# Kernel optimization log

Hardware: AMD Instinct MI355X
Metric: run time of the kernel (lower is better)

The kernel has to match this reference:

```python
import jax, jax.numpy as jnp
import numpy as np

EPS = 1e-6
B, T, D, A = 16, 2048, 512, 128
SCALE = A ** (-0.5)


def _xavier(key, fan_in, fan_out):
    limit = np.sqrt(6.0 / (fan_in + fan_out)).astype(np.float32)
    return jax.random.uniform(key, (fan_in, fan_out), jnp.float32, -limit, limit)


def setup_inputs() -> dict:
    key = jax.random.key(0)
    kx, kq, kk, kv = jax.random.split(key, 4)
    x = jax.random.normal(kx, (B, T, D), jnp.float32)
    Wq = _xavier(kq, D, A)
    Wk = _xavier(kk, D, A)
    Wv = _xavier(kv, D, 1)
    bq = jnp.full((A,), 0.01, jnp.float32)
    bk = jnp.full((A,), 0.01, jnp.float32)
    bv = jnp.full((1,), 0.01, jnp.float32)
    return {"x": x, "Wq": Wq, "bq": bq, "Wk": Wk, "bk": bk, "Wv": Wv, "bv": bv}


def reference(x, Wq, bq, Wk, bk, Wv, bv):
    # mean-variance norm over features (torch.std default is unbiased -> ddof=1)
    mu = jnp.mean(x, axis=-1, keepdims=True)
    sd = jnp.std(x, axis=-1, keepdims=True, ddof=1)
    xn = (x - mu) / (sd + EPS)
    Q = xn @ Wq + bq            # [B, T, A]
    K = xn @ Wk + bk            # [B, T, A]
    V = xn @ Wv + bv            # [B, T, 1]
    scores = jnp.einsum("bta,bsa->bts", Q, K) * SCALE  # [B, T, T]
    w_att = jax.nn.softmax(scores, axis=-1)
    w = jnp.einsum("bts,bso->bto", w_att, V)           # [B, T, 1]
    return (w, w_att)
```

## Files before the change

kernel.cpp:

```cpp
#include <hip/hip_runtime.h>

#define NB 16
#define NT 2048
#define ND 512
#define NA 128
#define EPSV 1e-6f
#define SCALE 0.08838834764831845f
#define NCH 4
#define SCH 512

typedef __bf16 bf16;
typedef __bf16 bf16x4 __attribute__((ext_vector_type(4)));
typedef __bf16 bf16x8 __attribute__((ext_vector_type(8)));
typedef float f32x4 __attribute__((ext_vector_type(4)));

__global__ void prep_wt(const float* __restrict__ Wq, const float* __restrict__ Wk,
                        bf16* __restrict__ WT) {
    int n = blockIdx.x;
    const float* W = (n < NA) ? Wq : Wk;
    int col = n & (NA - 1);
    for (int k = threadIdx.x; k < ND; k += blockDim.x)
        WT[(size_t)n * ND + k] = (bf16)W[(size_t)k * NA + col];
}

__launch_bounds__(256)
__global__ void norm_proj(const float* __restrict__ x, const float* __restrict__ Wv,
                          const float* __restrict__ bvp, const bf16* __restrict__ WT,
                          const float* __restrict__ bq, const float* __restrict__ bk,
                          bf16* __restrict__ QK, float* __restrict__ Vout) {
    __shared__ bf16 xn[16 * ND];
    const int tid = threadIdx.x;
    const int lane = tid & 63, wv = tid >> 6;
    const int row0 = blockIdx.x * 16;

    float wvv[8];
    float sumw = 0.f;
#pragma unroll
    for (int i = 0; i < 4; ++i) { wvv[i]     = Wv[lane * 4 + i];       sumw += wvv[i]; }
#pragma unroll
    for (int i = 0; i < 4; ++i) { wvv[4 + i] = Wv[256 + lane * 4 + i]; sumw += wvv[4 + i]; }
#pragma unroll
    for (int m = 1; m < 64; m <<= 1) sumw += __shfl_xor(sumw, m);
    const float bvs = bvp[0];

#pragma unroll
    for (int r = 0; r < 4; ++r) {
        const int lrow = wv * 4 + r;
        const int grow = row0 + lrow;
        const float* xr = x + (size_t)grow * ND;
        f32x4 a = *(const f32x4*)(xr + lane * 4);
        f32x4 b = *(const f32x4*)(xr + 256 + lane * 4);
        float s = 0.f, sq = 0.f, dw = 0.f;
#pragma unroll
        for (int i = 0; i < 4; ++i) { s += a[i]; sq += a[i] * a[i]; dw += a[i] * wvv[i]; }
#pragma unroll
        for (int i = 0; i < 4; ++i) { s += b[i]; sq += b[i] * b[i]; dw += b[i] * wvv[4 + i]; }
#pragma unroll
        for (int m = 1; m < 64; m <<= 1) {
            s  += __shfl_xor(s, m);
            sq += __shfl_xor(sq, m);
            dw += __shfl_xor(dw, m);
        }
        const float mu  = s * (1.f / 512.f);
        float var = (sq - 512.f * mu * mu) * (1.f / 511.f);
        var = fmaxf(var, 0.f);
        const float inv = 1.f / (sqrtf(var) + EPSV);
        if (lane == 0) Vout[grow] = (dw - mu * sumw) * inv + bvs;

        const int sw = (lrow & 7) << 4;
        bf16x4 v0, v1;
#pragma unroll
        for (int i = 0; i < 4; ++i) v0[i] = (bf16)((a[i] - mu) * inv);
#pragma unroll
        for (int i = 0; i < 4; ++i) v1[i] = (bf16)((b[i] - mu) * inv);
        *(bf16x4*)((char*)xn + lrow * 1024 + ((lane * 8) ^ sw))       = v0;
        *(bf16x4*)((char*)xn + lrow * 1024 + ((512 + lane * 8) ^ sw)) = v1;
    }
    __syncthreads();

    const int c = lane & 15, g = lane >> 4;
    const int asw = (c & 7) << 4;
    f32x4 acc[4];
#pragma unroll
    for (int i = 0; i < 4; ++i) acc[i] = f32x4{0.f, 0.f, 0.f, 0.f};

    for (int ks = 0; ks < 16; ++ks) {
        const bf16x8 af = *(const bf16x8*)((const char*)xn + c * 1024 +
                                           ((ks * 64 + g * 16) ^ asw));
#pragma unroll
        for (int i = 0; i < 4; ++i) {
            const int n = wv * 64 + i * 16 + c;
            const bf16x8 bfr = *(const bf16x8*)(WT + (size_t)n * ND + ks * 32 + g * 8);
            acc[i] = __builtin_amdgcn_mfma_f32_16x16x32_bf16(af, bfr, acc[i], 0, 0, 0);
        }
    }
#pragma unroll
    for (int i = 0; i < 4; ++i) {
        const int n = wv * 64 + i * 16 + c;
        const float bias = (n < NA) ? bq[n] : bk[n - NA];
#pragma unroll
        for (int j = 0; j < 4; ++j)
            QK[(size_t)(row0 + g * 4 + j) * 256 + n] = (bf16)(acc[i][j] + bias);
    }
}

__launch_bounds__(256, 3)
__global__ void attn_pass1(const bf16* __restrict__ QK, const float* __restrict__ Vg,
                           float* __restrict__ pl, float* __restrict__ pw) {
    __shared__ float redl[4][64], redw[4][64];
    const int tid = threadIdx.x;
    const int lane = tid & 63, w = tid >> 6;
    const int b = blockIdx.z, t0 = blockIdx.x * 64, sc = blockIdx.y;
    const int c = lane & 15, g = lane >> 4;

    bf16x8 qf[4][4];
#pragma unroll
    for (int tb = 0; tb < 4; ++tb) {
        const bf16* qrow = QK + (size_t)(b * NT + t0 + tb * 16 + c) * 256;
#pragma unroll
        for (int ks = 0; ks < 4; ++ks)
            qf[tb][ks] = *(const bf16x8*)(qrow + ks * 32 + g * 8);
    }

    const bf16* kp = QK + (size_t)(b * NT + sc * SCH + w * 16 + c) * 256 + NA + g * 8;
    const float* vp = Vg + b * NT + sc * SCH + w * 16 + g * 4;

    bf16x8 kf[4], kfn[4];
#pragma unroll
    for (int ks = 0; ks < 4; ++ks) kf[ks] = *(const bf16x8*)(kp + ks * 32);

    float l_loc[4] = {0.f, 0.f, 0.f, 0.f}, w_loc[4] = {0.f, 0.f, 0.f, 0.f};

    for (int tt = 0; tt < SCH / 64; ++tt) {
        if (tt + 1 < SCH / 64) {
#pragma unroll
            for (int ks = 0; ks < 4; ++ks)
                kfn[ks] = *(const bf16x8*)(kp + (size_t)(tt + 1) * 64 * 256 + ks * 32);
        }
        const f32x4 vv = *(const f32x4*)(vp + tt * 64);
        f32x4 acc[4];
#pragma unroll
        for (int tb = 0; tb < 4; ++tb) acc[tb] = f32x4{0.f, 0.f, 0.f, 0.f};
#pragma unroll
        for (int tb = 0; tb < 4; ++tb)
#pragma unroll
            for (int ks = 0; ks < 4; ++ks)
                acc[tb] = __builtin_amdgcn_mfma_f32_16x16x32_bf16(kf[ks], qf[tb][ks],
                                                                  acc[tb], 0, 0, 0);
#pragma unroll
        for (int tb = 0; tb < 4; ++tb)
#pragma unroll
            for (int jj = 0; jj < 4; ++jj) {
                const float p = __expf(acc[tb][jj] * SCALE);
                l_loc[tb] += p;
                w_loc[tb] += p * vv[jj];
            }
#pragma unroll
        for (int ks = 0; ks < 4; ++ks) kf[ks] = kfn[ks];
    }

#pragma unroll
    for (int tb = 0; tb < 4; ++tb) {
#pragma unroll
        for (int mask = 16; mask <= 32; mask <<= 1) {
            l_loc[tb] += __shfl_xor(l_loc[tb], mask);
            w_loc[tb] += __shfl_xor(w_loc[tb], mask);
        }
    }
    if (g == 0) {
#pragma unroll
        for (int tb = 0; tb < 4; ++tb) {
            redl[w][tb * 16 + c] = l_loc[tb];
            redw[w][tb * 16 + c] = w_loc[tb];
        }
    }
    __syncthreads();
    if (tid < 64) {
        float L = 0.f, W = 0.f;
#pragma unroll
        for (int ww = 0; ww < 4; ++ww) { L += redl[ww][tid]; W += redw[ww][tid]; }
        const int idx = sc * (NB * NT) + b * NT + t0 + tid;
        pl[idx] = L;
        pw[idx] = W;
    }
}

__global__ void attn_reduce(const float* __restrict__ pl, const float* __restrict__ pw,
                            float* __restrict__ linv, float* __restrict__ out_w) {
    const int r = blockIdx.x * 256 + threadIdx.x;
    float L = 0.f, W = 0.f;
#pragma unroll
    for (int ch = 0; ch < NCH; ++ch) {
        L += pl[ch * (NB * NT) + r];
        W += pw[ch * (NB * NT) + r];
    }
    linv[r] = 1.f / L;
    out_w[r] = W / L;
}

__launch_bounds__(256, 3)
__global__ void attn_pass2(const bf16* __restrict__ QK, const float* __restrict__ linv,
                           float* __restrict__ out_att) {
    const int tid = threadIdx.x;
    const int lane = tid & 63, w = tid >> 6;
    const int b = blockIdx.z, t0 = blockIdx.x * 64, sc = blockIdx.y;
    const int c = lane & 15, g = lane >> 4;

    bf16x8 qf[4][4];
    float li[4];
#pragma unroll
    for (int tb = 0; tb < 4; ++tb) {
        const bf16* qrow = QK + (size_t)(b * NT + t0 + tb * 16 + c) * 256;
#pragma unroll
        for (int ks = 0; ks < 4; ++ks)
            qf[tb][ks] = *(const bf16x8*)(qrow + ks * 32 + g * 8);
        li[tb] = linv[b * NT + t0 + tb * 16 + c];
    }

    const bf16* kp = QK + (size_t)(b * NT + sc * SCH + w * 16 + c) * 256 + NA + g * 8;

    bf16x8 kf[4], kfn[4];
#pragma unroll
    for (int ks = 0; ks < 4; ++ks) kf[ks] = *(const bf16x8*)(kp + ks * 32);

    float* obase = out_att + (size_t)(b * NT) * NT + sc * SCH + w * 16 + g * 4;

    for (int tt = 0; tt < SCH / 64; ++tt) {
        if (tt + 1 < SCH / 64) {
#pragma unroll
            for (int ks = 0; ks < 4; ++ks)
                kfn[ks] = *(const bf16x8*)(kp + (size_t)(tt + 1) * 64 * 256 + ks * 32);
        }
        f32x4 acc[4];
#pragma unroll
        for (int tb = 0; tb < 4; ++tb) acc[tb] = f32x4{0.f, 0.f, 0.f, 0.f};
#pragma unroll
        for (int tb = 0; tb < 4; ++tb)
#pragma unroll
            for (int ks = 0; ks < 4; ++ks)
                acc[tb] = __builtin_amdgcn_mfma_f32_16x16x32_bf16(kf[ks], qf[tb][ks],
                                                                  acc[tb], 0, 0, 0);
#pragma unroll
        for (int tb = 0; tb < 4; ++tb) {
            f32x4 wv4;
#pragma unroll
            for (int jj = 0; jj < 4; ++jj)
                wv4[jj] = __expf(acc[tb][jj] * SCALE) * li[tb];
            *(f32x4*)(obase + (size_t)(t0 + tb * 16 + c) * NT + tt * 64) = wv4;
        }
#pragma unroll
        for (int ks = 0; ks < 4; ++ks) kf[ks] = kfn[ks];
    }
}

extern "C" void kernel_launch(void* const* d_in, const int* in_sizes, int n_in,
                              void* d_out, int out_size, void* d_ws, size_t ws_size,
                              hipStream_t stream) {
    const float* x  = (const float*)d_in[0];
    const float* Wq = (const float*)d_in[1];
    const float* bq = (const float*)d_in[2];
    const float* Wk = (const float*)d_in[3];
    const float* bk = (const float*)d_in[4];
    const float* Wv = (const float*)d_in[5];
    const float* bv = (const float*)d_in[6];

    float* out_w   = (float*)d_out;
    float* out_att = (float*)d_out + NB * NT;

    char* ws = (char*)d_ws;
    bf16*  WT   = (bf16*)ws;
    float* V    = (float*)(ws + 262144);
    bf16*  QK   = (bf16*)(ws + 393216);
    float* pl   = (float*)(ws + 17170432);
    float* pw   = (float*)(ws + 17694720);
    float* linv = (float*)(ws + 18219008);

    prep_wt<<<dim3(256), dim3(256), 0, stream>>>(Wq, Wk, WT);
    norm_proj<<<dim3((NB * NT) / 16), dim3(256), 0, stream>>>(x, Wv, bv, WT, bq, bk, QK, V);
    attn_pass1<<<dim3(NT / 64, NCH, NB), dim3(256), 0, stream>>>(QK, V, pl, pw);
    attn_reduce<<<dim3((NB * NT) / 256), dim3(256), 0, stream>>>(pl, pw, linv, out_w);
    attn_pass2<<<dim3(NT / 64, NCH, NB), dim3(256), 0, stream>>>(QK, linv, out_att);
}
```

Measured before the change: 207.8 us.

## Stage K tiles through double-buffered swizzled LDS in attention passes

Both attention passes now load each 64-row K tile cooperatively with coalesced 16-byte global reads into a double-buffered, XOR-swizzled shared-memory buffer, then read MFMA fragments from LDS. Previously each lane loaded its fragment straight from global memory with a strided pattern. This adds 32 KB of LDS per block and a barrier every iteration, and drops the occupancy hint of 3 blocks per CU from the launch bounds.

After: 191.5 us. -7.8%, faster.

```diff
diff --git a/kernel.cpp b/kernel.cpp
--- a/kernel.cpp
+++ b/kernel.cpp
@@ -104,9 +104,10 @@
     }
 }
 
-__launch_bounds__(256, 3)
+__launch_bounds__(256)
 __global__ void attn_pass1(const bf16* __restrict__ QK, const float* __restrict__ Vg,
                            float* __restrict__ pl, float* __restrict__ pw) {
+    __shared__ bf16 Kt[2][64 * NA];
     __shared__ float redl[4][64], redw[4][64];
     const int tid = threadIdx.x;
     const int lane = tid & 63, w = tid >> 6;
@@ -122,31 +123,45 @@
             qf[tb][ks] = *(const bf16x8*)(qrow + ks * 32 + g * 8);
     }
 
-    const bf16* kp = QK + (size_t)(b * NT + sc * SCH + w * 16 + c) * 256 + NA + g * 8;
+    const int srow = tid >> 4, scc = tid & 15;
+    const bf16* kbase = QK + (size_t)(b * NT + sc * SCH + srow) * 256 + NA + scc * 8;
+    const int koff = srow * 256 + ((scc * 16) ^ ((srow & 7) << 4));
+    bf16x8 sreg[4];
+
+#pragma unroll
+    for (int i = 0; i < 4; ++i)
+        sreg[i] = *(const bf16x8*)(kbase + (size_t)(i * 16) * 256);
+#pragma unroll
+    for (int i = 0; i < 4; ++i)
+        *(bf16x8*)((char*)Kt[0] + koff + i * 4096) = sreg[i];
+    __syncthreads();
+
     const float* vp = Vg + b * NT + sc * SCH + w * 16 + g * 4;
-
-    bf16x8 kf[4], kfn[4];
-#pragma unroll
-    for (int ks = 0; ks < 4; ++ks) kf[ks] = *(const bf16x8*)(kp + ks * 32);
-
+    const int asw = (c & 7) << 4;
     float l_loc[4] = {0.f, 0.f, 0.f, 0.f}, w_loc[4] = {0.f, 0.f, 0.f, 0.f};
 
     for (int tt = 0; tt < SCH / 64; ++tt) {
         if (tt + 1 < SCH / 64) {
 #pragma unroll
+            for (int i = 0; i < 4; ++i)
+                sreg[i] = *(const bf16x8*)(kbase + (size_t)((tt + 1) * 64 + i * 16) * 256);
+        }
+        const char* ab = (const char*)Kt[tt & 1] + (w * 16 + c) * 256;
+        bf16x8 af[4];
+#pragma unroll
+        for (int ks = 0; ks < 4; ++ks)
+            af[ks] = *(const bf16x8*)(ab + ((ks * 64 + g * 16) ^ asw));
+
+        f32x4 acc[4];
+#pragma unroll
+        for (int tb = 0; tb < 4; ++tb) acc[tb] = f32x4{0.f, 0.f, 0.f, 0.f};
+#pragma unroll
+        for (int tb = 0; tb < 4; ++tb)
+#pragma unroll
             for (int ks = 0; ks < 4; ++ks)
-                kfn[ks] = *(const bf16x8*)(kp + (size_t)(tt + 1) * 64 * 256 + ks * 32);
-        }
+                acc[tb] = __builtin_amdgcn_mfma_f32_16x16x32_bf16(af[ks], qf[tb][ks],
+                                                                  acc[tb], 0, 0, 0);
         const f32x4 vv = *(const f32x4*)(vp + tt * 64);
-        f32x4 acc[4];
-#pragma unroll
-        for (int tb = 0; tb < 4; ++tb) acc[tb] = f32x4{0.f, 0.f, 0.f, 0.f};
-#pragma unroll
-        for (int tb = 0; tb < 4; ++tb)
-#pragma unroll
-            for (int ks = 0; ks < 4; ++ks)
-                acc[tb] = __builtin_amdgcn_mfma_f32_16x16x32_bf16(kf[ks], qf[tb][ks],
-                                                                  acc[tb], 0, 0, 0);
 #pragma unroll
         for (int tb = 0; tb < 4; ++tb)
 #pragma unroll
@@ -155,8 +170,12 @@
                 l_loc[tb] += p;
                 w_loc[tb] += p * vv[jj];
             }
-#pragma unroll
-        for (int ks = 0; ks < 4; ++ks) kf[ks] = kfn[ks];
+        if (tt + 1 < SCH / 64) {
+#pragma unroll
+            for (int i = 0; i < 4; ++i)
+                *(bf16x8*)((char*)Kt[(tt + 1) & 1] + koff + i * 4096) = sreg[i];
+        }
+        __syncthreads();
     }
 
 #pragma unroll
@@ -198,9 +217,10 @@
     out_w[r] = W / L;
 }
 
-__launch_bounds__(256, 3)
+__launch_bounds__(256)
 __global__ void attn_pass2(const bf16* __restrict__ QK, const float* __restrict__ linv,
                            float* __restrict__ out_att) {
+    __shared__ bf16 Kt[2][64 * NA];
     const int tid = threadIdx.x;
     const int lane = tid & 63, w = tid >> 6;
     const int b = blockIdx.z, t0 = blockIdx.x * 64, sc = blockIdx.y;
@@ -217,28 +237,42 @@
         li[tb] = linv[b * NT + t0 + tb * 16 + c];
     }
 
-    const bf16* kp = QK + (size_t)(b * NT + sc * SCH + w * 16 + c) * 256 + NA + g * 8;
-
-    bf16x8 kf[4], kfn[4];
-#pragma unroll
-    for (int ks = 0; ks < 4; ++ks) kf[ks] = *(const bf16x8*)(kp + ks * 32);
-
+    const int srow = tid >> 4, scc = tid & 15;
+    const bf16* kbase = QK + (size_t)(b * NT + sc * SCH + srow) * 256 + NA + scc * 8;
+    const int koff = srow * 256 + ((scc * 16) ^ ((srow & 7) << 4));
+    bf16x8 sreg[4];
+
+#pragma unroll
+    for (int i = 0; i < 4; ++i)
+        sreg[i] = *(const bf16x8*)(kbase + (size_t)(i * 16) * 256);
+#pragma unroll
+    for (int i = 0; i < 4; ++i)
+        *(bf16x8*)((char*)Kt[0] + koff + i * 4096) = sreg[i];
+    __syncthreads();
+
+    const int asw = (c & 7) << 4;
     float* obase = out_att + (size_t)(b * NT) * NT + sc * SCH + w * 16 + g * 4;
 
     for (int tt = 0; tt < SCH / 64; ++tt) {
         if (tt + 1 < SCH / 64) {
 #pragma unroll
+            for (int i = 0; i < 4; ++i)
+                sreg[i] = *(const bf16x8*)(kbase + (size_t)((tt + 1) * 64 + i * 16) * 256);
+        }
+        const char* ab = (const char*)Kt[tt & 1] + (w * 16 + c) * 256;
+        bf16x8 af[4];
+#pragma unroll
+        for (int ks = 0; ks < 4; ++ks)
+            af[ks] = *(const bf16x8*)(ab + ((ks * 64 + g * 16) ^ asw));
+
+        f32x4 acc[4];
+#pragma unroll
+        for (int tb = 0; tb < 4; ++tb) acc[tb] = f32x4{0.f, 0.f, 0.f, 0.f};
+#pragma unroll
+        for (int tb = 0; tb < 4; ++tb)
+#pragma unroll
             for (int ks = 0; ks < 4; ++ks)
-                kfn[ks] = *(const bf16x8*)(kp + (size_t)(tt + 1) * 64 * 256 + ks * 32);
-        }
-        f32x4 acc[4];
-#pragma unroll
-        for (int tb = 0; tb < 4; ++tb) acc[tb] = f32x4{0.f, 0.f, 0.f, 0.f};
-#pragma unroll
-        for (int tb = 0; tb < 4; ++tb)
-#pragma unroll
-            for (int ks = 0; ks < 4; ++ks)
-                acc[tb] = __builtin_amdgcn_mfma_f32_16x16x32_bf16(kf[ks], qf[tb][ks],
+                acc[tb] = __builtin_amdgcn_mfma_f32_16x16x32_bf16(af[ks], qf[tb][ks],
                                                                   acc[tb], 0, 0, 0);
 #pragma unroll
         for (int tb = 0; tb < 4; ++tb) {
@@ -248,8 +282,12 @@
                 wv4[jj] = __expf(acc[tb][jj] * SCALE) * li[tb];
             *(f32x4*)(obase + (size_t)(t0 + tb * 16 + c) * NT + tt * 64) = wv4;
         }
-#pragma unroll
-        for (int ks = 0; ks < 4; ++ks) kf[ks] = kfn[ks];
+        if (tt + 1 < SCH / 64) {
+#pragma unroll
+            for (int i = 0; i < 4; ++i)
+                *(bf16x8*)((char*)Kt[(tt + 1) & 1] + koff + i * 4096) = sreg[i];
+        }
+        __syncthreads();
     }
 }
 
```
